# Kernel tuning notes

Hardware: AMD Instinct MI355X
Metric: run time of the kernel (lower is better)

## Reference

```python
import jax, jax.numpy as jnp
import numpy as np

DIM = 4096
N_HEADS = 32
HEAD_DIM = DIM // N_HEADS
BATCH = 2
SEQ = 1024
THETA = 10000.0
NEG_INF = -1e9


def _rope_cos_sin(seq_len, head_dim):
    # NOTE: original code constructs RotatePosEmbedding with config.dim but applies
    # it per-head; the only shape-consistent interpretation (standard Llama RoPE)
    # uses head_dim frequencies, which is what we implement.
    inv_freq = 1.0 / (THETA ** (jnp.arange(0, head_dim, 2, dtype=jnp.float32) / head_dim))
    angles = jnp.arange(seq_len, dtype=jnp.float32)[:, None] * inv_freq[None, :]  # [S, hd/2]
    return jnp.cos(angles), jnp.sin(angles)


def _apply_rope(x, cos, sin):
    # x: [B,S,H,hd]; rotate consecutive pairs (complex multiply)
    B, S, H, hd = x.shape
    xr = x.reshape(B, S, H, hd // 2, 2)
    x0, x1 = xr[..., 0], xr[..., 1]
    c = cos[None, :, None, :]
    s = sin[None, :, None, :]
    out = jnp.stack([x0 * c - x1 * s, x0 * s + x1 * c], axis=-1)
    return out.reshape(B, S, H, hd)


def setup_inputs() -> dict:
    key = jax.random.key(0)
    ks = jax.random.split(key, 9)
    x = jax.random.normal(ks[0], (BATCH, SEQ, DIM), dtype=jnp.float32)
    scale = 1.0 / np.sqrt(DIM)
    wq = jax.random.normal(ks[1], (DIM, DIM), dtype=jnp.float32) * scale
    wk = jax.random.normal(ks[2], (DIM, DIM), dtype=jnp.float32) * scale
    wv = jax.random.normal(ks[3], (DIM, DIM), dtype=jnp.float32) * scale
    wo = jax.random.normal(ks[4], (DIM, DIM), dtype=jnp.float32) * scale
    bq = jax.random.normal(ks[5], (DIM,), dtype=jnp.float32) * 0.01
    bk = jax.random.normal(ks[6], (DIM,), dtype=jnp.float32) * 0.01
    bv = jax.random.normal(ks[7], (DIM,), dtype=jnp.float32) * 0.01
    bo = jax.random.normal(ks[8], (DIM,), dtype=jnp.float32) * 0.01
    # causal additive mask [S,S]
    mask = jnp.where(jnp.tril(jnp.ones((SEQ, SEQ), dtype=bool)), 0.0, NEG_INF).astype(jnp.float32)
    return {"x": x, "wq": wq, "bq": bq, "wk": wk, "bk": bk, "wv": wv, "bv": bv,
            "wo": wo, "bo": bo, "mask": mask, "start_pos": 0}


def reference(x, wq, bq, wk, bk, wv, bv, wo, bo, mask, start_pos):
    B, S, D = x.shape
    H, hd = N_HEADS, D // N_HEADS
    q = (x @ wq.T + bq).reshape(B, S, H, hd)
    k = (x @ wk.T + bk).reshape(B, S, H, hd)
    v = (x @ wv.T + bv).reshape(B, S, H, hd)
    cos, sin = _rope_cos_sin(S, hd)
    q = _apply_rope(q, cos, sin)
    k = _apply_rope(k, cos, sin)
    # start_pos == 0 prefill: cache slice [:start_pos+S] equals current k/v
    scores = jnp.einsum('bqhd,bkhd->bhqk', q, k) / np.sqrt(hd).astype(np.float32)
    scores = scores + mask[None, None, :, :]
    attn = jax.nn.softmax(scores, axis=-1)
    out = jnp.einsum('bhqk,bkhd->bqhd', attn, v).reshape(B, S, D)
    return out @ wo.T + bo
```

## Files before the change

### kernel.cpp

```cpp
#include <hip/hip_runtime.h>
#include <hip/hip_bf16.h>

#define DIM   4096
#define NH    32
#define HD    128
#define BATCH 2
#define SEQ   1024
#define MROWS (BATCH*SEQ)
#define LDQ   12288

typedef __attribute__((ext_vector_type(8))) short bf16x8;
typedef __attribute__((ext_vector_type(4))) short s16x4;
typedef __attribute__((ext_vector_type(4))) float f32x4;

__device__ inline void gload_lds16(const void* g, void* l) {
  __builtin_amdgcn_global_load_lds(
      (const __attribute__((address_space(1))) void*)g,
      (__attribute__((address_space(3))) void*)l, 16, 0, 0);
}

__device__ inline float bf2f(short b) {
  unsigned u = ((unsigned)(unsigned short)b) << 16;
  return __uint_as_float(u);
}
__device__ inline unsigned short f2bfu(float f) {
  __hip_bfloat16 h = __float2bfloat16(f);
  return *reinterpret_cast<unsigned short*>(&h);
}

template <int N> __device__ __forceinline__ void wait_vm() {
  if constexpr (N == 0)      asm volatile("s_waitcnt vmcnt(0)" ::: "memory");
  else if constexpr (N == 4) asm volatile("s_waitcnt vmcnt(4)" ::: "memory");
  else                       asm volatile("s_waitcnt vmcnt(8)" ::: "memory");
}

__global__ void cvt_bf16_kernel(const float* __restrict__ in,
                                unsigned short* __restrict__ out, long n4) {
  long i = blockIdx.x * (long)blockDim.x + threadIdx.x;
  long stride = (long)gridDim.x * blockDim.x;
  for (; i < n4; i += stride) {
    float4 v = ((const float4*)in)[i];
    ushort4 o;
    o.x = f2bfu(v.x); o.y = f2bfu(v.y); o.z = f2bfu(v.z); o.w = f2bfu(v.w);
    ((ushort4*)out)[i] = o;
  }
}

__global__ void concat3_kernel(const float* __restrict__ a, const float* __restrict__ b,
                               const float* __restrict__ c, float* __restrict__ o) {
  int i = blockIdx.x * blockDim.x + threadIdx.x;
  if (i < 4096) o[i] = a[i];
  else if (i < 8192) o[i] = b[i - 4096];
  else if (i < 12288) o[i] = c[i - 8192];
}

__global__ void rope_table_kernel(float* __restrict__ cosT, float* __restrict__ sinT) {
  int s = blockIdx.x;
  int p = threadIdx.x;
  float inv = powf(10000.0f, -((float)(2 * p)) / 128.0f);
  float a = (float)s * inv;
  cosT[s * 64 + p] = cosf(a);
  sinT[s * 64 + p] = sinf(a);
}

__global__ void reduce_bias_kernel(const float* __restrict__ part,
                                   const float* __restrict__ bias,
                                   float* __restrict__ out) {
  long i = blockIdx.x * (long)blockDim.x + threadIdx.x;
  if (i >= (long)MROWS * DIM / 4) return;
  float4 a = ((const float4*)part)[i];
  float4 b = ((const float4*)(part + (size_t)MROWS * DIM))[i];
  float4 bb = ((const float4*)bias)[(int)(i & (DIM / 4 - 1))];
  float4 o;
  o.x = a.x + b.x + bb.x; o.y = a.y + b.y + bb.y;
  o.z = a.z + b.z + bb.z; o.w = a.w + b.w + bb.w;
  ((float4*)out)[i] = o;
}

template <typename OutT, bool QKV_MODE>
__global__ __launch_bounds__(512, 2) void gemm_v3_kernel(
    const unsigned short* __restrict__ A, const unsigned short* __restrict__ Bw,
    const float* __restrict__ bias, OutT* __restrict__ C,
    int M, int N, int Kstr, int Klen,
    const float* __restrict__ cosT, const float* __restrict__ sinT) {
  __shared__ unsigned short As[4][256 * 32];
  __shared__ unsigned short Bs[4][256 * 32];
  const int t = threadIdx.x;
  const int lane = t & 63;
  const int w = t >> 6;
  const int wm = w >> 2, wn = w & 3;
  const int np = lane & 15, hq = lane >> 4;

  int bid = blockIdx.y * gridDim.x + blockIdx.x;
  int nwg = gridDim.x * gridDim.y;
  int sb = (bid & 7) * (nwg >> 3) + (bid >> 3);
  int bx = sb % gridDim.x, by = sb / gridDim.x;
  const int m0 = by * 256, n0 = bx * 256;
  const int kb0 = blockIdx.z * Klen;
  const int NT = Klen >> 5;
  OutT* Cz = C + (size_t)blockIdx.z * (size_t)M * N;

  auto stage = [&](int slot, int kcol0) {
#pragma unroll
    for (int j = 0; j < 2; ++j) {
      int ci = j * 512 + t;
      int r = ci >> 2, cg = (ci & 3) ^ ((r >> 1) & 3);
      gload_lds16(A + (size_t)(m0 + r) * Kstr + kcol0 + cg * 8, &As[slot][ci * 8]);
    }
#pragma unroll
    for (int j = 0; j < 2; ++j) {
      int ci = j * 512 + t;
      int r = ci >> 2, cg = (ci & 3) ^ ((r >> 1) & 3);
      gload_lds16(Bw + (size_t)(n0 + r) * Kstr + kcol0 + cg * 8, &Bs[slot][ci * 8]);
    }
  };

  stage(0, kb0); stage(1, kb0 + 32); stage(2, kb0 + 64);

  f32x4 acc[8][4] = {};

  wait_vm<8>();
  __builtin_amdgcn_s_barrier();

#pragma unroll 1
  for (int u = 0; u < NT; ++u) {
    const unsigned short* Asl = As[u & 3];
    const unsigned short* Bsl = Bs[u & 3];
    const int cswz = (np >> 1) & 3;
    const int kc = (hq ^ cswz) << 3;
    bf16x8 af[8], bf[4];
#pragma unroll
    for (int i = 0; i < 4; ++i)
      af[i] = *(const bf16x8*)&Asl[(wm * 128 + i * 16 + np) * 32 + kc];
#pragma unroll
    for (int j = 0; j < 4; ++j)
      bf[j] = *(const bf16x8*)&Bsl[(wn * 64 + j * 16 + np) * 32 + kc];
#pragma unroll
    for (int i = 4; i < 8; ++i)
      af[i] = *(const bf16x8*)&Asl[(wm * 128 + i * 16 + np) * 32 + kc];

    if (u + 3 < NT) stage((u + 3) & 3, kb0 + ((u + 3) << 5));

    __builtin_amdgcn_s_setprio(1);
#pragma unroll
    for (int i = 0; i < 4; ++i)
#pragma unroll
      for (int j = 0; j < 4; ++j)
        acc[i][j] = __builtin_amdgcn_mfma_f32_16x16x32_bf16(af[i], bf[j], acc[i][j], 0, 0, 0);
    __builtin_amdgcn_s_setprio(0);
    __builtin_amdgcn_s_setprio(1);
#pragma unroll
    for (int i = 4; i < 8; ++i)
#pragma unroll
      for (int j = 0; j < 4; ++j)
        acc[i][j] = __builtin_amdgcn_mfma_f32_16x16x32_bf16(af[i], bf[j], acc[i][j], 0, 0, 0);
    __builtin_amdgcn_s_setprio(0);

    if (u + 3 < NT)      wait_vm<8>();
    else if (u + 2 < NT) wait_vm<4>();
    else                 wait_vm<0>();
    __builtin_amdgcn_s_barrier();
  }

  const int orow0 = m0 + wm * 128;
  const int ocol0 = n0 + wn * 64 + np;
#pragma unroll
  for (int j = 0; j < 4; ++j) {
    const int col = ocol0 + j * 16;
    float bj = QKV_MODE ? bias[col] : 0.0f;
    const int p0 = (col & 127) >> 1;
    const bool even = (lane & 1) == 0;
    const bool do_rope = QKV_MODE && (col < 8192);
#pragma unroll
    for (int i = 0; i < 8; ++i) {
#pragma unroll
      for (int r = 0; r < 4; ++r) {
        int orow = orow0 + i * 16 + hq * 4 + r;
        float v = acc[i][j][r] + bj;
        float pv = __shfl_xor(v, 1);
        if (do_rope) {
          int srow = orow & (SEQ - 1);
          float c = cosT[srow * 64 + p0];
          float s = sinT[srow * 64 + p0];
          v = even ? (v * c - pv * s) : (pv * s + v * c);
        }
        size_t off = (size_t)orow * N + col;
        if constexpr (sizeof(OutT) == 2)
          ((unsigned short*)Cz)[off] = f2bfu(v);
        else
          ((float*)Cz)[off] = v;
      }
    }
  }
}

__global__ __launch_bounds__(256, 1) void flash_attn_kernel(
    const unsigned short* __restrict__ QKV, unsigned short* __restrict__ O) {
  __shared__ unsigned short Ks[64 * 128];
  __shared__ unsigned short Vt[128 * 64];
  __shared__ unsigned short Ps[4][32 * 64];

  const int p  = blockIdx.x;
  const int bh = blockIdx.y;
  const int b  = bh >> 5;
  const int hh = bh & 31;
  const int t    = threadIdx.x;
  const int lane = t & 63;
  const int w    = t >> 6;
  const int np   = lane & 15;
  const int hq   = lane >> 4;

  const size_t rowbase = (size_t)b * SEQ * LDQ;
  const unsigned short* Qg = QKV + rowbase + (size_t)hh * HD;
  const unsigned short* Kg = QKV + rowbase + 4096 + (size_t)hh * HD;
  const unsigned short* Vg = QKV + rowbase + 8192 + (size_t)hh * HD;
  unsigned short* Og = O + (size_t)b * SEQ * DIM + (size_t)hh * HD;

  const int krow = t >> 2;
  const int kc0  = (t & 3) * 32;
  const int vr0  = (t & 15) * 4;
  const int vc0  = (t >> 4) * 8;

  unsigned short* Pw = &Ps[w][0];
  const float SCALE = 0.08838834764831843f;

  bf16x8 vk[4], vv[4];

#pragma unroll 1
  for (int pass = 0; pass < 2; ++pass) {
    const int qt    = pass ? (7 - p) : p;
    const int nt    = 2 * qt + 2;
    const int qbase = qt * 128 + w * 32;

    bf16x8 qf[2][4];
#pragma unroll
    for (int rb = 0; rb < 2; ++rb)
#pragma unroll
      for (int kb = 0; kb < 4; ++kb)
        qf[rb][kb] = *(const bf16x8*)&Qg[(size_t)(qbase + rb * 16 + np) * LDQ + kb * 32 + hq * 8];

    f32x4 acc[2][8] = {};
    float m_run[2][4], l_run[2][4];
#pragma unroll
    for (int rb = 0; rb < 2; ++rb)
#pragma unroll
      for (int r = 0; r < 4; ++r) { m_run[rb][r] = -3.0e38f; l_run[rb][r] = 0.0f; }

    {
      const unsigned short* kp = Kg + (size_t)krow * LDQ + kc0;
      const unsigned short* vp = Vg + (size_t)vr0 * LDQ + vc0;
#pragma unroll
      for (int jj = 0; jj < 4; ++jj) vk[jj] = *(const bf16x8*)(kp + jj * 8);
#pragma unroll
      for (int jj = 0; jj < 4; ++jj) vv[jj] = *(const bf16x8*)(vp + (size_t)jj * LDQ);
    }

#pragma unroll 1
    for (int kt = 0; kt < nt; ++kt) {
      __syncthreads();

#pragma unroll
      for (int jj = 0; jj < 4; ++jj) {
        int c = (t & 3) * 4 + jj;
        *(bf16x8*)((char*)Ks + krow * 256 + ((c ^ (krow & 7)) << 4)) = vk[jj];
      }
#pragma unroll
      for (int i = 0; i < 8; ++i) {
        int col = vc0 + i;
        s16x4 sv;
        sv[0] = vv[0][i]; sv[1] = vv[1][i]; sv[2] = vv[2][i]; sv[3] = vv[3][i];
        *(s16x4*)((char*)Vt + ((col * 128 + vr0 * 2) ^ ((col & 7) << 4))) = sv;
      }
      __syncthreads();

      if (kt + 1 < nt) {
        const unsigned short* kp = Kg + (size_t)((kt + 1) * 64 + krow) * LDQ + kc0;
        const unsigned short* vp = Vg + (size_t)((kt + 1) * 64 + vr0) * LDQ + vc0;
#pragma unroll
        for (int jj = 0; jj < 4; ++jj) vk[jj] = *(const bf16x8*)(kp + jj * 8);
#pragma unroll
        for (int jj = 0; jj < 4; ++jj) vv[jj] = *(const bf16x8*)(vp + (size_t)jj * LDQ);
      }

      f32x4 sc[4][2] = {};
#pragma unroll
      for (int ct = 0; ct < 4; ++ct) {
#pragma unroll
        for (int kb = 0; kb < 4; ++kb) {
          bf16x8 kf = *(const bf16x8*)((char*)Ks + (ct * 16 + np) * 256 +
                                       (((kb * 4 + hq) ^ (np & 7)) << 4));
          sc[ct][0] = __builtin_amdgcn_mfma_f32_16x16x32_bf16(qf[0][kb], kf, sc[ct][0], 0, 0, 0);
          sc[ct][1] = __builtin_amdgcn_mfma_f32_16x16x32_bf16(qf[1][kb], kf, sc[ct][1], 0, 0, 0);
        }
      }

      const bool maskt = (kt >= 2 * qt);
#pragma unroll
      for (int ct = 0; ct < 4; ++ct) {
        int kvc = kt * 64 + ct * 16 + np;
#pragma unroll
        for (int rb = 0; rb < 2; ++rb)
#pragma unroll
          for (int r = 0; r < 4; ++r) {
            float v = sc[ct][rb][r] * SCALE;
            if (maskt && kvc > qbase + rb * 16 + hq * 4 + r) v = -1.0e9f;
            sc[ct][rb][r] = v;
          }
      }

      float sf[2][4];
#pragma unroll
      for (int rb = 0; rb < 2; ++rb)
#pragma unroll
        for (int r = 0; r < 4; ++r) {
          float tmax = fmaxf(fmaxf(sc[0][rb][r], sc[1][rb][r]),
                             fmaxf(sc[2][rb][r], sc[3][rb][r]));
          tmax = fmaxf(tmax, __shfl_xor(tmax, 1));
          tmax = fmaxf(tmax, __shfl_xor(tmax, 2));
          tmax = fmaxf(tmax, __shfl_xor(tmax, 4));
          tmax = fmaxf(tmax, __shfl_xor(tmax, 8));
          float mn = fmaxf(m_run[rb][r], tmax);
          sf[rb][r] = __expf(m_run[rb][r] - mn);
          m_run[rb][r] = mn;
        }

#pragma unroll
      for (int rb = 0; rb < 2; ++rb)
#pragma unroll
        for (int r = 0; r < 4; ++r) {
          int prow = rb * 16 + hq * 4 + r;
          int swz = (prow & 7) << 4;
          float rsum = 0.f;
#pragma unroll
          for (int ct = 0; ct < 4; ++ct) {
            float pv = __expf(sc[ct][rb][r] - m_run[rb][r]);
            rsum += pv;
            *(unsigned short*)((char*)Pw + ((prow * 128 + (ct * 16 + np) * 2) ^ swz)) = f2bfu(pv);
          }
          rsum += __shfl_xor(rsum, 1);
          rsum += __shfl_xor(rsum, 2);
          rsum += __shfl_xor(rsum, 4);
          rsum += __shfl_xor(rsum, 8);
          l_run[rb][r] = l_run[rb][r] * sf[rb][r] + rsum;
        }

#pragma unroll
      for (int rb = 0; rb < 2; ++rb)
#pragma unroll
        for (int nt2 = 0; nt2 < 8; ++nt2)
#pragma unroll
          for (int r = 0; r < 4; ++r)
            acc[rb][nt2][r] *= sf[rb][r];

#pragma unroll
      for (int kb2 = 0; kb2 < 2; ++kb2) {
        bf16x8 pa0 = *(const bf16x8*)((char*)Pw +
            (((0 * 16 + np) * 128 + kb2 * 64 + hq * 16) ^ ((np & 7) << 4)));
        bf16x8 pa1 = *(const bf16x8*)((char*)Pw +
            (((1 * 16 + np) * 128 + kb2 * 64 + hq * 16) ^ ((np & 7) << 4)));
#pragma unroll
        for (int nt2 = 0; nt2 < 8; ++nt2) {
          int col = nt2 * 16 + np;
          bf16x8 vf = *(const bf16x8*)((char*)Vt +
              ((col * 128 + kb2 * 64 + hq * 16) ^ ((col & 7) << 4)));
          acc[0][nt2] = __builtin_amdgcn_mfma_f32_16x16x32_bf16(pa0, vf, acc[0][nt2], 0, 0, 0);
          acc[1][nt2] = __builtin_amdgcn_mfma_f32_16x16x32_bf16(pa1, vf, acc[1][nt2], 0, 0, 0);
        }
      }
    }

#pragma unroll
    for (int rb = 0; rb < 2; ++rb)
#pragma unroll
      for (int r = 0; r < 4; ++r) {
        float rl = 1.0f / l_run[rb][r];
        int orow = qbase + rb * 16 + hq * 4 + r;
#pragma unroll
        for (int nt2 = 0; nt2 < 8; ++nt2)
          Og[(size_t)orow * DIM + nt2 * 16 + np] = f2bfu(acc[rb][nt2][r] * rl);
      }
  }
}

extern "C" void kernel_launch(void* const* d_in, const int* in_sizes, int n_in,
                              void* d_out, int out_size, void* d_ws, size_t ws_size,
                              hipStream_t stream) {
  const float* x  = (const float*)d_in[0];
  const float* wq = (const float*)d_in[1];
  const float* bq = (const float*)d_in[2];
  const float* wk = (const float*)d_in[3];
  const float* bk = (const float*)d_in[4];
  const float* wv = (const float*)d_in[5];
  const float* bv = (const float*)d_in[6];
  const float* wo = (const float*)d_in[7];
  const float* bo = (const float*)d_in[8];
  float* out = (float*)d_out;

  char* ws = (char*)d_ws;
  unsigned short* wqkvb = (unsigned short*)(ws);
  float* part           = (float*)(ws);
  unsigned short* wob   = (unsigned short*)(ws + (96ll  << 20));
  unsigned short* xb    = (unsigned short*)(ws + (128ll << 20));
  unsigned short* qkv   = (unsigned short*)(ws + (144ll << 20));
  unsigned short* ab    = (unsigned short*)(ws + (192ll << 20));
  float* biasqkv = (float*)(ws + (208ll << 20));
  float* cosT    = (float*)(ws + (208ll << 20) + (64  << 10));
  float* sinT    = (float*)(ws + (208ll << 20) + (320 << 10));

  cvt_bf16_kernel<<<2048, 256, 0, stream>>>(x,  xb, (long)MROWS * DIM / 4);
  cvt_bf16_kernel<<<2048, 256, 0, stream>>>(wq, wqkvb,                        (long)DIM * DIM / 4);
  cvt_bf16_kernel<<<2048, 256, 0, stream>>>(wk, wqkvb + (size_t)DIM * DIM,    (long)DIM * DIM / 4);
  cvt_bf16_kernel<<<2048, 256, 0, stream>>>(wv, wqkvb + 2 * (size_t)DIM * DIM,(long)DIM * DIM / 4);
  cvt_bf16_kernel<<<2048, 256, 0, stream>>>(wo, wob, (long)DIM * DIM / 4);

  concat3_kernel<<<48, 256, 0, stream>>>(bq, bk, bv, biasqkv);
  rope_table_kernel<<<SEQ, 64, 0, stream>>>(cosT, sinT);

  dim3 gq(LDQ / 256, MROWS / 256, 1);
  gemm_v3_kernel<unsigned short, true><<<gq, 512, 0, stream>>>(
      xb, wqkvb, biasqkv, qkv, MROWS, LDQ, DIM, DIM, cosT, sinT);

  dim3 ga(4, BATCH * NH);
  flash_attn_kernel<<<ga, 256, 0, stream>>>(qkv, ab);

  dim3 go(DIM / 256, MROWS / 256, 2);
  gemm_v3_kernel<float, false><<<go, 512, 0, stream>>>(
      ab, wob, nullptr, part, MROWS, DIM, DIM, DIM / 2, nullptr, nullptr);

  reduce_bias_kernel<<<(MROWS * DIM / 4 + 255) / 256, 256, 0, stream>>>(part, bo, out);
}
```

Baseline: 533.6 us.

## Restructure GEMM main loop into double-buffered 64-wide K steps with interleaved staging

Replaces the 4-slot, 32-wide K ring buffer in the bf16 GEMM with two 64-wide buffers, each split into two 32-wide halves. Every iteration computes in four phases (A/B halves × N halves), and each phase issues one slice of the next tile's global-to-LDS loads. The aim is to spread memory traffic evenly across the MFMA work and halve the number of outer loop iterations. In exchange it adds more barriers per iteration and leaves a shallower prefetch distance than the previous three-tile-ahead scheme.

```diff
diff --git a/kernel.cpp b/kernel.cpp
--- a/kernel.cpp
+++ b/kernel.cpp
@@ -30,8 +30,7 @@
 
 template <int N> __device__ __forceinline__ void wait_vm() {
   if constexpr (N == 0)      asm volatile("s_waitcnt vmcnt(0)" ::: "memory");
-  else if constexpr (N == 4) asm volatile("s_waitcnt vmcnt(4)" ::: "memory");
-  else                       asm volatile("s_waitcnt vmcnt(8)" ::: "memory");
+  else                       asm volatile("s_waitcnt vmcnt(4)" ::: "memory");
 }
 
 __global__ void cvt_bf16_kernel(const float* __restrict__ in,
@@ -78,18 +77,20 @@
 }
 
 template <typename OutT, bool QKV_MODE>
-__global__ __launch_bounds__(512, 2) void gemm_v3_kernel(
+__global__ __launch_bounds__(512, 2) void gemm_kh_kernel(
     const unsigned short* __restrict__ A, const unsigned short* __restrict__ Bw,
     const float* __restrict__ bias, OutT* __restrict__ C,
     int M, int N, int Kstr, int Klen,
     const float* __restrict__ cosT, const float* __restrict__ sinT) {
-  __shared__ unsigned short As[4][256 * 32];
-  __shared__ unsigned short Bs[4][256 * 32];
+  __shared__ unsigned short As[2][2][256 * 32];
+  __shared__ unsigned short Bs[2][2][256 * 32];
   const int t = threadIdx.x;
   const int lane = t & 63;
   const int w = t >> 6;
   const int wm = w >> 2, wn = w & 3;
   const int np = lane & 15, hq = lane >> 4;
+  const int rsw = (np >> 1) & 3;
+  const int kc = (hq ^ rsw) << 3;
 
   int bid = blockIdx.y * gridDim.x + blockIdx.x;
   int nwg = gridDim.x * gridDim.y;
@@ -97,69 +98,103 @@
   int bx = sb % gridDim.x, by = sb / gridDim.x;
   const int m0 = by * 256, n0 = bx * 256;
   const int kb0 = blockIdx.z * Klen;
-  const int NT = Klen >> 5;
+  const int NT = Klen >> 6;
   OutT* Cz = C + (size_t)blockIdx.z * (size_t)M * N;
 
-  auto stage = [&](int slot, int kcol0) {
+  auto stageAk = [&](int bsel, int kh, int kcol0) {
 #pragma unroll
     for (int j = 0; j < 2; ++j) {
       int ci = j * 512 + t;
-      int r = ci >> 2, cg = (ci & 3) ^ ((r >> 1) & 3);
-      gload_lds16(A + (size_t)(m0 + r) * Kstr + kcol0 + cg * 8, &As[slot][ci * 8]);
-    }
+      int r = ci >> 2, p = ci & 3, g = p ^ ((r >> 1) & 3);
+      gload_lds16(A + (size_t)(m0 + r) * Kstr + kcol0 + kh * 32 + g * 8,
+                  &As[bsel][kh][ci * 8]);
+    }
+  };
+  auto stageBk = [&](int bsel, int kh, int kcol0) {
 #pragma unroll
     for (int j = 0; j < 2; ++j) {
       int ci = j * 512 + t;
-      int r = ci >> 2, cg = (ci & 3) ^ ((r >> 1) & 3);
-      gload_lds16(Bw + (size_t)(n0 + r) * Kstr + kcol0 + cg * 8, &Bs[slot][ci * 8]);
+      int r = ci >> 2, p = ci & 3, g = p ^ ((r >> 1) & 3);
+      gload_lds16(Bw + (size_t)(n0 + r) * Kstr + kcol0 + kh * 32 + g * 8,
+                  &Bs[bsel][kh][ci * 8]);
     }
   };
 
-  stage(0, kb0); stage(1, kb0 + 32); stage(2, kb0 + 64);
+  stageAk(0, 0, kb0); stageBk(0, 0, kb0);
+  stageAk(0, 1, kb0); stageBk(0, 1, kb0);
+  wait_vm<4>();
+  __builtin_amdgcn_s_barrier();
 
   f32x4 acc[8][4] = {};
-
-  wait_vm<8>();
-  __builtin_amdgcn_s_barrier();
 
 #pragma unroll 1
   for (int u = 0; u < NT; ++u) {
-    const unsigned short* Asl = As[u & 3];
-    const unsigned short* Bsl = Bs[u & 3];
-    const int cswz = (np >> 1) & 3;
-    const int kc = (hq ^ cswz) << 3;
-    bf16x8 af[8], bf[4];
-#pragma unroll
-    for (int i = 0; i < 4; ++i)
-      af[i] = *(const bf16x8*)&Asl[(wm * 128 + i * 16 + np) * 32 + kc];
-#pragma unroll
-    for (int j = 0; j < 4; ++j)
-      bf[j] = *(const bf16x8*)&Bsl[(wn * 64 + j * 16 + np) * 32 + kc];
-#pragma unroll
-    for (int i = 4; i < 8; ++i)
-      af[i] = *(const bf16x8*)&Asl[(wm * 128 + i * 16 + np) * 32 + kc];
-
-    if (u + 3 < NT) stage((u + 3) & 3, kb0 + ((u + 3) << 5));
-
+    const int cb_ = u & 1, nb = cb_ ^ 1;
+    const int kn = kb0 + ((u + 1) << 6);
+    const bool more = (u + 1 < NT);
+    bf16x8 af[8], bfr[4];
+
+#pragma unroll
+    for (int i = 0; i < 8; ++i)
+      af[i] = *(const bf16x8*)&As[cb_][0][(wm * 128 + i * 16 + np) * 32 + kc];
+#pragma unroll
+    for (int j = 0; j < 2; ++j)
+      bfr[j] = *(const bf16x8*)&Bs[cb_][0][(wn * 64 + j * 16 + np) * 32 + kc];
+    if (more) stageAk(nb, 0, kn);
     __builtin_amdgcn_s_setprio(1);
 #pragma unroll
-    for (int i = 0; i < 4; ++i)
-#pragma unroll
-      for (int j = 0; j < 4; ++j)
-        acc[i][j] = __builtin_amdgcn_mfma_f32_16x16x32_bf16(af[i], bf[j], acc[i][j], 0, 0, 0);
+    for (int i = 0; i < 8; ++i)
+#pragma unroll
+      for (int j = 0; j < 2; ++j)
+        acc[i][j] = __builtin_amdgcn_mfma_f32_16x16x32_bf16(af[i], bfr[j], acc[i][j], 0, 0, 0);
     __builtin_amdgcn_s_setprio(0);
+    __builtin_amdgcn_s_barrier();
+
+#pragma unroll
+    for (int j = 0; j < 2; ++j)
+      bfr[2 + j] = *(const bf16x8*)&Bs[cb_][0][(wn * 64 + 32 + j * 16 + np) * 32 + kc];
+    if (more) stageBk(nb, 0, kn);
     __builtin_amdgcn_s_setprio(1);
 #pragma unroll
-    for (int i = 4; i < 8; ++i)
-#pragma unroll
-      for (int j = 0; j < 4; ++j)
-        acc[i][j] = __builtin_amdgcn_mfma_f32_16x16x32_bf16(af[i], bf[j], acc[i][j], 0, 0, 0);
+    for (int i = 0; i < 8; ++i)
+#pragma unroll
+      for (int j = 2; j < 4; ++j)
+        acc[i][j] = __builtin_amdgcn_mfma_f32_16x16x32_bf16(af[i], bfr[j], acc[i][j], 0, 0, 0);
     __builtin_amdgcn_s_setprio(0);
-
-    if (u + 3 < NT)      wait_vm<8>();
-    else if (u + 2 < NT) wait_vm<4>();
-    else                 wait_vm<0>();
+    if (more) wait_vm<4>(); else wait_vm<0>();
     __builtin_amdgcn_s_barrier();
+
+#pragma unroll
+    for (int i = 0; i < 8; ++i)
+      af[i] = *(const bf16x8*)&As[cb_][1][(wm * 128 + i * 16 + np) * 32 + kc];
+#pragma unroll
+    for (int j = 0; j < 2; ++j)
+      bfr[j] = *(const bf16x8*)&Bs[cb_][1][(wn * 64 + j * 16 + np) * 32 + kc];
+    if (more) stageAk(nb, 1, kn);
+    __builtin_amdgcn_s_setprio(1);
+#pragma unroll
+    for (int i = 0; i < 8; ++i)
+#pragma unroll
+      for (int j = 0; j < 2; ++j)
+        acc[i][j] = __builtin_amdgcn_mfma_f32_16x16x32_bf16(af[i], bfr[j], acc[i][j], 0, 0, 0);
+    __builtin_amdgcn_s_setprio(0);
+    __builtin_amdgcn_s_barrier();
+
+#pragma unroll
+    for (int j = 0; j < 2; ++j)
+      bfr[2 + j] = *(const bf16x8*)&Bs[cb_][1][(wn * 64 + 32 + j * 16 + np) * 32 + kc];
+    if (more) stageBk(nb, 1, kn);
+    __builtin_amdgcn_s_setprio(1);
+#pragma unroll
+    for (int i = 0; i < 8; ++i)
+#pragma unroll
+      for (int j = 2; j < 4; ++j)
+        acc[i][j] = __builtin_amdgcn_mfma_f32_16x16x32_bf16(af[i], bfr[j], acc[i][j], 0, 0, 0);
+    __builtin_amdgcn_s_setprio(0);
+    if (more) {
+      wait_vm<4>();
+      __builtin_amdgcn_s_barrier();
+    }
   }
 
   const int orow0 = m0 + wm * 128;
@@ -417,14 +452,14 @@
   rope_table_kernel<<<SEQ, 64, 0, stream>>>(cosT, sinT);
 
   dim3 gq(LDQ / 256, MROWS / 256, 1);
-  gemm_v3_kernel<unsigned short, true><<<gq, 512, 0, stream>>>(
+  gemm_kh_kernel<unsigned short, true><<<gq, 512, 0, stream>>>(
       xb, wqkvb, biasqkv, qkv, MROWS, LDQ, DIM, DIM, cosT, sinT);
 
   dim3 ga(4, BATCH * NH);
   flash_attn_kernel<<<ga, 256, 0, stream>>>(qkv, ab);
 
   dim3 go(DIM / 256, MROWS / 256, 2);
-  gemm_v3_kernel<float, false><<<go, 512, 0, stream>>>(
+  gemm_kh_kernel<float, false><<<go, 512, 0, stream>>>(
       ab, wob, nullptr, part, MROWS, DIM, DIM, DIM / 2, nullptr, nullptr);
 
   reduce_bias_kernel<<<(MROWS * DIM / 4 + 255) / 256, 256, 0, stream>>>(part, bo, out);
```

New measurement: 543.6 us. No clear change (+1.9%).
